# Kernel optimization log

Measured on AMD Instinct MI355X. Metric: run time of the kernel, lower is better.

Reference implementation:

```python
import jax, jax.numpy as jnp
import numpy as np

K = 3      # fixed 3x3 kernel in module
PAD = 1    # padding=1, stride=1, dilation=1, groups=1, deformable_groups=1


def _conv2d(x, w, b=None, pad=PAD):
    out = jax.lax.conv_general_dilated(
        x, w, window_strides=(1, 1), padding=((pad, pad), (pad, pad)),
        dimension_numbers=('NCHW', 'OIHW', 'NCHW'))
    if b is not None:
        out = out + b[None, :, None, None]
    return out


def _bilinear_gather(x, py, px):
    # x: [B,C,H,W]; py,px: [B,KK,H,W] float sampling coords (zero-pad outside)
    B, C, H, W = x.shape
    y0 = jnp.floor(py)
    x0 = jnp.floor(px)
    wy1 = py - y0
    wx1 = px - x0
    wy0 = 1.0 - wy1
    wx0 = 1.0 - wx1
    y0i = y0.astype(jnp.int32)
    x0i = x0.astype(jnp.int32)
    xf = x.reshape(B, C, H * W)

    def corner(yi, xi, w):
        valid = (yi >= 0) & (yi < H) & (xi >= 0) & (xi < W)
        yc = jnp.clip(yi, 0, H - 1)
        xc = jnp.clip(xi, 0, W - 1)
        idx = (yc * W + xc).reshape(B, -1)                     # [B, KK*H*W]
        v = jnp.take_along_axis(xf, idx[:, None, :], axis=2)  # [B, C, KK*H*W]
        return v * (w * valid).reshape(B, 1, -1)

    out = (corner(y0i,     x0i,     wy0 * wx0)
         + corner(y0i,     x0i + 1, wy0 * wx1)
         + corner(y0i + 1, x0i,     wy1 * wx0)
         + corner(y0i + 1, x0i + 1, wy1 * wx1))
    KK = py.shape[1]
    return out.reshape(B, C, KK, H, W)


def _deform_forward(x, offset_w, offset_b, conv_w):
    B, C, H, W = x.shape
    # offset branch: plain 3x3 conv -> [B, 2*K*K, H, W], layout (k, (dy,dx))
    off = _conv2d(x, offset_w, offset_b).reshape(B, K * K, 2, H, W)
    ys = jnp.arange(H, dtype=x.dtype)
    xs = jnp.arange(W, dtype=x.dtype)
    ky, kx = jnp.meshgrid(jnp.arange(K), jnp.arange(K), indexing='ij')
    ky = ky.reshape(-1).astype(x.dtype)   # [9]
    kx = kx.reshape(-1).astype(x.dtype)
    # sampling coords p = p0 + p_k + offset   -> [B, 9, H, W]
    py = ys[None, None, :, None] - PAD + ky[None, :, None, None] + off[:, :, 0]
    px = xs[None, None, None, :] - PAD + kx[None, :, None, None] + off[:, :, 1]
    sampled = _bilinear_gather(x, py, px)                       # [B,C,9,H,W]
    O = conv_w.shape[0]
    return jnp.einsum('bckhw,ock->bohw', sampled, conv_w.reshape(O, C, K * K))


def setup_inputs() -> dict:
    key = jax.random.key(0)
    k1, k2, k3 = jax.random.split(key, 3)
    B, C, O, H, W = 8, 256, 256, 64, 64
    x = jax.random.normal(k1, (B, C, H, W), dtype=jnp.float32)
    # small random offset weights so learned offsets are ~ +/- 2 px
    offset_w = jax.random.normal(k2, (2 * K * K, C, K, K), dtype=jnp.float32) * 0.05
    offset_b = jnp.zeros((2 * K * K,), dtype=jnp.float32)
    conv_w = jax.random.normal(k3, (O, C, K, K), dtype=jnp.float32) * 0.02
    return {"x": x, "offset_w": offset_w, "offset_b": offset_b, "conv_w": conv_w}


def reference(x, offset_w, offset_b, conv_w):
    return _deform_forward(x, offset_w, offset_b, conv_w)
```

## Files before the change

kernel.cpp:

```cpp
#include <hip/hip_runtime.h>

using short8 = __attribute__((ext_vector_type(8))) short;
using f32x4  = __attribute__((ext_vector_type(4))) float;

__device__ inline unsigned short f2bf(float f) {
  unsigned u = __float_as_uint(f);
  u += 0x7fffu + ((u >> 16) & 1u);
  return (unsigned short)(u >> 16);
}
__device__ inline float bf2f(short s) {
  return __uint_as_float(((unsigned)(unsigned short)s) << 16);
}

__device__ inline void barrier_lgkm() {
  asm volatile("s_waitcnt lgkmcnt(0)\n\ts_barrier" ::: "memory");
}

__global__ __launch_bounds__(256) void prep_all(
    const float* __restrict__ x, const float* __restrict__ cw,
    const float* __restrict__ ow, unsigned short* __restrict__ xT,
    unsigned short* __restrict__ xTlo, unsigned short* __restrict__ wBt2,
    unsigned short* __restrict__ wOt, unsigned short* __restrict__ wOtLo) {
  __shared__ float tile[32 * 268];
  int bid = blockIdx.x, tid = threadIdx.x;
  if (bid < 1024) {
    int xh = bid & 1, y = (bid >> 1) & 63, b = bid >> 7;
    int xc = tid & 31, cq = tid >> 5;
#pragma unroll 4
    for (int i = 0; i < 32; ++i) {
      int c = i * 8 + cq;
      tile[xc * 268 + c] =
          x[(((size_t)((b << 8) + c)) << 12) + (y << 6) + xh * 32 + xc];
    }
    __syncthreads();
#pragma unroll 2
    for (int i = 0; i < 8; ++i) {
      int u = i * 256 + tid;
      int site = u >> 6, c4 = u & 63;
      float4 v = *(const float4*)(tile + site * 268 + c4 * 4);
      ushort4 hi, lo;
      hi.x = f2bf(v.x); lo.x = f2bf(v.x - bf2f(hi.x));
      hi.y = f2bf(v.y); lo.y = f2bf(v.y - bf2f(hi.y));
      hi.z = f2bf(v.z); lo.z = f2bf(v.z - bf2f(hi.z));
      hi.w = f2bf(v.w); lo.w = f2bf(v.w - bf2f(hi.w));
      size_t addr = (((size_t)((b << 12) + (y << 6) + xh * 32 + site)) << 8) + c4 * 4;
      *(ushort4*)(xT + addr) = hi;
      *(ushort4*)(xTlo + addr) = lo;
    }
  } else if (bid < 3328) {
    int e = (bid - 1024) * 256 + tid;
    int kc = e & 31, o = (e >> 5) & 255, ks = e >> 13;
    int c = (ks & 7) * 32 + kc, kt = ks >> 3;
    wBt2[e] = f2bf(cw[(size_t)(o * 256 + c) * 9 + kt]);
  } else {
    int e = (bid - 3328) * 256 + tid;
    int kc = e & 31, o = (e >> 5) & 31, ks = e >> 10;
    int c = (ks & 7) * 32 + kc, kt = ks >> 3;
    float v = (o < 18) ? ow[(size_t)(o * 256 + c) * 9 + kt] : 0.f;
    unsigned short hi = f2bf(v);
    wOt[e] = hi;
    wOtLo[e] = f2bf(v - bf2f(hi));
  }
}

__device__ inline void gatherOff2(const unsigned short* xT, const unsigned short* xTlo,
                                  const unsigned short* zp, int b, int h, int p16,
                                  int q, int ccg, int ky, int kx,
                                  short8* gh, short8* gl) {
  int y = h + ky - 1;
  bool yv = (unsigned)y < 64u;
  int yc = min(max(y, 0), 63);
#pragma unroll
  for (int i = 0; i < 4; ++i) {
    int px = i * 16 + p16;
    int xx = px + kx - 1;
    bool v = yv && ((unsigned)xx < 64u);
    int xc = min(max(xx, 0), 63);
    size_t base = (((size_t)((b << 12) + (yc << 6) + xc)) << 8) + ccg * 32 + q * 8;
    const unsigned short* ph = v ? (xT + base) : zp;
    const unsigned short* pl = v ? (xTlo + base) : zp;
    gh[i] = *(const short8*)ph;
    gl[i] = *(const short8*)pl;
  }
}
__device__ inline void loadBOff2(const unsigned short* wOt, const unsigned short* wOtLo,
                                 int ks, int m16, int quad, short8* bh, short8* bl) {
  const unsigned short* bp = wOt + (ks << 10) + m16 * 32 + quad * 8;
  const unsigned short* bq = wOtLo + (ks << 10) + m16 * 32 + quad * 8;
  bh[0] = *(const short8*)bp;  bh[1] = *(const short8*)(bp + 512);
  bl[0] = *(const short8*)bq;  bl[1] = *(const short8*)(bq + 512);
}

__global__ __launch_bounds__(64) void offset_conv3(
    const unsigned short* __restrict__ xT, const unsigned short* __restrict__ xTlo,
    const unsigned short* __restrict__ wOt, const unsigned short* __restrict__ wOtLo,
    const unsigned short* __restrict__ zp, float* out) {
  __shared__ unsigned short Ah[2 * 2560], Al[2 * 2560];
  int lane = threadIdx.x;
  int bid = blockIdx.x;
  int b = bid & 7, h = (bid >> 3) & 63, ccq = bid >> 9;
  int m16 = lane & 15, quad = lane >> 4;
  int p16 = lane >> 2, q = lane & 3;
  f32x4 acc[4][2];
#pragma unroll
  for (int mt = 0; mt < 4; ++mt)
#pragma unroll
    for (int j = 0; j < 2; ++j) acc[mt][j] = (f32x4){0.f, 0.f, 0.f, 0.f};

  short8 gh[4], gl[4], bh[2], bl[2];
  gatherOff2(xT, xTlo, zp, b, h, p16, q, ccq, 0, 0, gh, gl);
  loadBOff2(wOt, wOtLo, ccq, m16, quad, bh, bl);

  for (int it = 0; it < 9; ++it) {
    int buf = it & 1;
#pragma unroll
    for (int i = 0; i < 4; ++i) {
      int px = i * 16 + p16;
      *(short8*)(Ah + buf * 2560 + px * 40 + q * 8) = gh[i];
      *(short8*)(Al + buf * 2560 + px * 40 + q * 8) = gl[i];
    }
    int jn = (it < 8) ? it + 1 : 8;
    int kyn = jn / 3, kxn = jn - kyn * 3;
    short8 ghn[4], gln[4], bhn[2], bln[2];
    loadBOff2(wOt, wOtLo, jn * 8 + ccq, m16, quad, bhn, bln);
    gatherOff2(xT, xTlo, zp, b, h, p16, q, ccq, kyn, kxn, ghn, gln);
#pragma unroll
    for (int mt = 0; mt < 4; ++mt) {
      short8 ah = *(const short8*)(Ah + buf * 2560 + (mt * 16 + m16) * 40 + quad * 8);
      short8 al = *(const short8*)(Al + buf * 2560 + (mt * 16 + m16) * 40 + quad * 8);
#pragma unroll
      for (int j = 0; j < 2; ++j) {
        acc[mt][j] = __builtin_amdgcn_mfma_f32_16x16x32_bf16(ah, bh[j], acc[mt][j], 0, 0, 0);
        acc[mt][j] = __builtin_amdgcn_mfma_f32_16x16x32_bf16(al, bh[j], acc[mt][j], 0, 0, 0);
        acc[mt][j] = __builtin_amdgcn_mfma_f32_16x16x32_bf16(ah, bl[j], acc[mt][j], 0, 0, 0);
      }
    }
#pragma unroll
    for (int i = 0; i < 4; ++i) { gh[i] = ghn[i]; gl[i] = gln[i]; }
    bh[0] = bhn[0]; bh[1] = bhn[1]; bl[0] = bln[0]; bl[1] = bln[1];
  }
#pragma unroll
  for (int j = 0; j < 2; ++j) {
    int o = j * 16 + m16;
    if (o < 18) {
      float* po = out + (((size_t)((b << 8) + 100 + ccq * 18 + o)) << 12) + (h << 6);
#pragma unroll
      for (int mt = 0; mt < 4; ++mt)
#pragma unroll
        for (int rr = 0; rr < 4; ++rr)
          po[mt * 16 + quad * 4 + rr] = acc[mt][j][rr];
    }
  }
}

__device__ inline void gather4(const unsigned short* __restrict__ xT,
                               int bbase, int q, int jt,
                               const int2* cif2, const float4* cwf4,
                               int px, short8* g, float4& wq) {
  int cc = jt / 9, kt = jt - cc * 9;
  int2 si = cif2[kt * 64 + px];
  wq = cwf4[kt * 64 + px];
  const unsigned short* base = xT + (size_t)(unsigned)(bbase + cc * 32 + q * 8);
  g[0] = *(const short8*)(base + si.x);
  g[1] = *(const short8*)(base + si.x + 256);
  g[2] = *(const short8*)(base + si.y);
  g[3] = *(const short8*)(base + si.y + 256);
}
__device__ inline void loadB(const unsigned short* __restrict__ wBt2, int wave,
                             int m16, int quad, int jt, short8* bf) {
  int cc = jt / 9, kt = jt - cc * 9;
  int ks = kt * 8 + cc;
  const unsigned short* bp =
      wBt2 + ((size_t)ks << 13) + (wave << 11) + m16 * 32 + quad * 8;
#pragma unroll
  for (int j = 0; j < 4; ++j)
    bf[j] = *(const short8*)(bp + j * 512);
}

__global__ __launch_bounds__(256, 2) void deform_main(
    const unsigned short* __restrict__ xT, const float* __restrict__ offb,
    const unsigned short* __restrict__ wBt2, float* out) {
  __shared__ float4 smem4[1504];
  char* smem = (char*)smem4;
  float4* cwf4 = (float4*)smem;
  int2*   cif2 = (int2*)(smem + 9216);
  unsigned short* At = (unsigned short*)(smem + 13824);

  int tid = threadIdx.x, lane = tid & 63, wave = tid >> 6;
  int b = blockIdx.x & 7, h = blockIdx.x >> 3;

  size_t bb = ((size_t)(b << 8)) << 12;
  for (int it = tid; it < 576; it += 256) {
    int k = it >> 6, px = it & 63;
    int ky = k / 3, kx = k - ky * 3;
    int idx = (h << 6) + px;
    float dy = offb[2 * k], dx = offb[2 * k + 1];
#pragma unroll
    for (int qq = 0; qq < 8; ++qq) {
      dy += out[bb + (((size_t)(100 + qq * 18 + 2 * k)) << 12) + idx];
      dx += out[bb + (((size_t)(101 + qq * 18 + 2 * k)) << 12) + idx];
    }
    float py = (float)(h - 1 + ky) + dy;
    float pxx = (float)(px - 1 + kx) + dx;
    float y0f = floorf(py), x0f = floorf(pxx);
    int y0 = (int)y0f, x0 = (int)x0f;
    float wy1 = py - y0f, wx1 = pxx - x0f;
    int xb; float wxl, wxr;
    if (x0 >= 0 && x0 <= 62)      { xb = x0; wxl = 1.f - wx1; wxr = wx1; }
    else if (x0 == -1)            { xb = 0;  wxl = wx1;       wxr = 0.f; }
    else if (x0 == 63)            { xb = 62; wxl = 0.f;       wxr = 1.f - wx1; }
    else                          { xb = 0;  wxl = 0.f;       wxr = 0.f; }
    float wy0v = ((unsigned)y0 < 64u) ? (1.f - wy1) : 0.f;
    float wy1v = ((unsigned)(y0 + 1) < 64u) ? wy1 : 0.f;
    int yc0 = min(max(y0, 0), 63), yc1 = min(max(y0 + 1, 0), 63);
    cwf4[it] = make_float4(wy0v * wxl, wy0v * wxr, wy1v * wxl, wy1v * wxr);
    cif2[it] = make_int2(((yc0 << 6) + xb) << 8, ((yc1 << 6) + xb) << 8);
  }
  __syncthreads();

  int m16 = lane & 15, quad = lane >> 4;
  int px = wave * 16 + (lane >> 2);
  int q  = lane & 3;
  int bbase = b << 20;
  f32x4 acc[4][4];
#pragma unroll
  for (int i = 0; i < 4; ++i)
#pragma unroll
    for (int j = 0; j < 4; ++j) acc[i][j] = (f32x4){0.f, 0.f, 0.f, 0.f};

  short8 g[4]; float4 wq; short8 bcur[4];
  gather4(xT, bbase, q, 0, cif2, cwf4, px, g, wq);
  loadB(wBt2, wave, m16, quad, 0, bcur);

  for (int it = 0; it < 72; ++it) {
    int buf = it & 1;
    short8 av;
#pragma unroll
    for (int i = 0; i < 8; ++i) {
      float v = wq.x * bf2f(g[0][i]) + wq.y * bf2f(g[1][i]) +
                wq.z * bf2f(g[2][i]) + wq.w * bf2f(g[3][i]);
      av[i] = (short)f2bf(v);
    }
    *(short8*)(At + buf * 2560 + px * 40 + q * 8) = av;
    int jn = (it < 71) ? it + 1 : 71;
    short8 bnext[4], gn[4]; float4 wqn;
    loadB(wBt2, wave, m16, quad, jn, bnext);
    gather4(xT, bbase, q, jn, cif2, cwf4, px, gn, wqn);
    barrier_lgkm();
    short8 af[4];
#pragma unroll
    for (int mt = 0; mt < 4; ++mt)
      af[mt] = *(const short8*)(At + buf * 2560 + (mt * 16 + m16) * 40 + quad * 8);
#pragma unroll
    for (int mt = 0; mt < 4; ++mt)
#pragma unroll
      for (int j = 0; j < 4; ++j)
        acc[mt][j] = __builtin_amdgcn_mfma_f32_16x16x32_bf16(af[mt], bcur[j],
                                                             acc[mt][j], 0, 0, 0);
#pragma unroll
    for (int i = 0; i < 4; ++i) g[i] = gn[i];
    wq = wqn;
#pragma unroll
    for (int j = 0; j < 4; ++j) bcur[j] = bnext[j];
  }

#pragma unroll
  for (int j = 0; j < 4; ++j) {
    int o = wave * 64 + j * 16 + m16;
    float* po = out + (((size_t)((b << 8) + o)) << 12) + (h << 6) + quad * 4;
#pragma unroll
    for (int mt = 0; mt < 4; ++mt) {
      float4 v = make_float4(acc[mt][j][0], acc[mt][j][1], acc[mt][j][2],
                             acc[mt][j][3]);
      *(float4*)(po + mt * 16) = v;
    }
  }
}

extern "C" void kernel_launch(void* const* d_in, const int* in_sizes, int n_in,
                              void* d_out, int out_size, void* d_ws, size_t ws_size,
                              hipStream_t stream) {
  const float* x     = (const float*)d_in[0];
  const float* offw  = (const float*)d_in[1];
  const float* offb  = (const float*)d_in[2];
  const float* convw = (const float*)d_in[3];
  float* out = (float*)d_out;

  char* ws = (char*)d_ws;
  unsigned short* wOt   = (unsigned short*)ws;
  unsigned short* wOtLo = (unsigned short*)(ws + 147456);
  unsigned short* wBt2  = (unsigned short*)(ws + 294912);
  unsigned short* xT    = (unsigned short*)(ws + 1474560);
  unsigned short* xTlo  = (unsigned short*)(ws + 18251776);
  const unsigned short* zp = wOt + 768;

  prep_all<<<3616, 256, 0, stream>>>(x, convw, offw, xT, xTlo, wBt2, wOt, wOtLo);
  offset_conv3<<<4096, 64, 0, stream>>>(xT, xTlo, wOt, wOtLo, zp, out);
  deform_main<<<512, 256, 0, stream>>>(xT, offb, wBt2, out);
}
```

Before: 185.5 us.

## Restructure offset conv to stage input rows in LDS and reduce channel splits in-block

```diff
diff --git a/kernel.cpp b/kernel.cpp
--- a/kernel.cpp
+++ b/kernel.cpp
@@ -63,26 +63,6 @@
   }
 }
 
-__device__ inline void gatherOff2(const unsigned short* xT, const unsigned short* xTlo,
-                                  const unsigned short* zp, int b, int h, int p16,
-                                  int q, int ccg, int ky, int kx,
-                                  short8* gh, short8* gl) {
-  int y = h + ky - 1;
-  bool yv = (unsigned)y < 64u;
-  int yc = min(max(y, 0), 63);
-#pragma unroll
-  for (int i = 0; i < 4; ++i) {
-    int px = i * 16 + p16;
-    int xx = px + kx - 1;
-    bool v = yv && ((unsigned)xx < 64u);
-    int xc = min(max(xx, 0), 63);
-    size_t base = (((size_t)((b << 12) + (yc << 6) + xc)) << 8) + ccg * 32 + q * 8;
-    const unsigned short* ph = v ? (xT + base) : zp;
-    const unsigned short* pl = v ? (xTlo + base) : zp;
-    gh[i] = *(const short8*)ph;
-    gl[i] = *(const short8*)pl;
-  }
-}
 __device__ inline void loadBOff2(const unsigned short* wOt, const unsigned short* wOtLo,
                                  int ks, int m16, int quad, short8* bh, short8* bl) {
   const unsigned short* bp = wOt + (ks << 10) + m16 * 32 + quad * 8;
@@ -91,64 +71,98 @@
   bl[0] = *(const short8*)bq;  bl[1] = *(const short8*)(bq + 512);
 }
 
-__global__ __launch_bounds__(64) void offset_conv3(
+__global__ __launch_bounds__(256) void offset_conv4(
     const unsigned short* __restrict__ xT, const unsigned short* __restrict__ xTlo,
     const unsigned short* __restrict__ wOt, const unsigned short* __restrict__ wOtLo,
-    const unsigned short* __restrict__ zp, float* out) {
-  __shared__ unsigned short Ah[2 * 2560], Al[2 * 2560];
-  int lane = threadIdx.x;
+    float* out) {
+  __shared__ unsigned short S[4 * 2 * 7920];
+  int tid = threadIdx.x, lane = tid & 63, wave = tid >> 6;
   int bid = blockIdx.x;
-  int b = bid & 7, h = (bid >> 3) & 63, ccq = bid >> 9;
+  int b = bid & 7, h = bid >> 3;
   int m16 = lane & 15, quad = lane >> 4;
-  int p16 = lane >> 2, q = lane & 3;
+  unsigned short* Sw = S + wave * 15840;
+
+  {
+    short8 z = (short8){0, 0, 0, 0, 0, 0, 0, 0};
+    if (lane < 48) {
+      int j = lane & 3, r = lane >> 2;
+      int buf = r >= 6; int rr = r - buf * 6; int ky = rr >> 1, pad = rr & 1;
+      int pxp = pad ? 65 : 0;
+      *(short8*)(Sw + buf * 7920 + (ky * 66 + pxp) * 40 + j * 8) = z;
+    }
+  }
+
   f32x4 acc[4][2];
 #pragma unroll
   for (int mt = 0; mt < 4; ++mt)
 #pragma unroll
     for (int j = 0; j < 2; ++j) acc[mt][j] = (f32x4){0.f, 0.f, 0.f, 0.f};
 
-  short8 gh[4], gl[4], bh[2], bl[2];
-  gatherOff2(xT, xTlo, zp, b, h, p16, q, ccq, 0, 0, gh, gl);
-  loadBOff2(wOt, wOtLo, ccq, m16, quad, bh, bl);
-
-  for (int it = 0; it < 9; ++it) {
-    int buf = it & 1;
-#pragma unroll
-    for (int i = 0; i < 4; ++i) {
-      int px = i * 16 + p16;
-      *(short8*)(Ah + buf * 2560 + px * 40 + q * 8) = gh[i];
-      *(short8*)(Al + buf * 2560 + px * 40 + q * 8) = gl[i];
-    }
-    int jn = (it < 8) ? it + 1 : 8;
-    int kyn = jn / 3, kxn = jn - kyn * 3;
-    short8 ghn[4], gln[4], bhn[2], bln[2];
-    loadBOff2(wOt, wOtLo, jn * 8 + ccq, m16, quad, bhn, bln);
-    gatherOff2(xT, xTlo, zp, b, h, p16, q, ccq, kyn, kxn, ghn, gln);
-#pragma unroll
-    for (int mt = 0; mt < 4; ++mt) {
-      short8 ah = *(const short8*)(Ah + buf * 2560 + (mt * 16 + m16) * 40 + quad * 8);
-      short8 al = *(const short8*)(Al + buf * 2560 + (mt * 16 + m16) * 40 + quad * 8);
-#pragma unroll
-      for (int j = 0; j < 2; ++j) {
-        acc[mt][j] = __builtin_amdgcn_mfma_f32_16x16x32_bf16(ah, bh[j], acc[mt][j], 0, 0, 0);
-        acc[mt][j] = __builtin_amdgcn_mfma_f32_16x16x32_bf16(al, bh[j], acc[mt][j], 0, 0, 0);
-        acc[mt][j] = __builtin_amdgcn_mfma_f32_16x16x32_bf16(ah, bl[j], acc[mt][j], 0, 0, 0);
+  for (int ci = 0; ci < 2; ++ci) {
+    int cc = wave + ci * 4;
+#pragma unroll
+    for (int ky = 0; ky < 3; ++ky) {
+      int y = h + ky - 1;
+      unsigned short* dh = Sw + (ky * 66 + lane + 1) * 40;
+      unsigned short* dl = dh + 7920;
+      if ((unsigned)y < 64u) {
+        size_t base = (((size_t)((b << 12) + (y << 6) + lane)) << 8) + cc * 32;
+        const unsigned short* sh_ = xT + base;
+        const unsigned short* sl_ = xTlo + base;
+#pragma unroll
+        for (int j = 0; j < 4; ++j) {
+          *(short8*)(dh + j * 8) = *(const short8*)(sh_ + j * 8);
+          *(short8*)(dl + j * 8) = *(const short8*)(sl_ + j * 8);
+        }
+      } else {
+        short8 z = (short8){0, 0, 0, 0, 0, 0, 0, 0};
+#pragma unroll
+        for (int j = 0; j < 4; ++j) {
+          *(short8*)(dh + j * 8) = z;
+          *(short8*)(dl + j * 8) = z;
+        }
       }
     }
-#pragma unroll
-    for (int i = 0; i < 4; ++i) { gh[i] = ghn[i]; gl[i] = gln[i]; }
-    bh[0] = bhn[0]; bh[1] = bhn[1]; bl[0] = bln[0]; bl[1] = bln[1];
-  }
+    for (int kt = 0; kt < 9; ++kt) {
+      int ky = kt / 3, kx = kt - ky * 3;
+      short8 bh[2], bl[2];
+      loadBOff2(wOt, wOtLo, kt * 8 + cc, m16, quad, bh, bl);
+#pragma unroll
+      for (int mt = 0; mt < 4; ++mt) {
+        const unsigned short* ap = Sw + (ky * 66 + mt * 16 + m16 + kx) * 40 + quad * 8;
+        short8 ah = *(const short8*)ap;
+        short8 al = *(const short8*)(ap + 7920);
+#pragma unroll
+        for (int j = 0; j < 2; ++j) {
+          acc[mt][j] = __builtin_amdgcn_mfma_f32_16x16x32_bf16(ah, bh[j], acc[mt][j], 0, 0, 0);
+          acc[mt][j] = __builtin_amdgcn_mfma_f32_16x16x32_bf16(al, bh[j], acc[mt][j], 0, 0, 0);
+          acc[mt][j] = __builtin_amdgcn_mfma_f32_16x16x32_bf16(ah, bl[j], acc[mt][j], 0, 0, 0);
+        }
+      }
+    }
+  }
+
+  __syncthreads();
+  float* red = (float*)S;
+#pragma unroll
+  for (int mt = 0; mt < 4; ++mt)
+#pragma unroll
+    for (int j = 0; j < 2; ++j)
+      *(f32x4*)(red + ((((wave * 4 + mt) * 2) + j) * 64 + lane) * 4) = acc[mt][j];
+  __syncthreads();
 #pragma unroll
   for (int j = 0; j < 2; ++j) {
     int o = j * 16 + m16;
+    f32x4 s = (f32x4){0.f, 0.f, 0.f, 0.f};
+#pragma unroll
+    for (int wv = 0; wv < 4; ++wv) {
+      f32x4 v = *(const f32x4*)(red + ((((wv * 4 + wave) * 2) + j) * 64 + lane) * 4);
+      s[0] += v[0]; s[1] += v[1]; s[2] += v[2]; s[3] += v[3];
+    }
     if (o < 18) {
-      float* po = out + (((size_t)((b << 8) + 100 + ccq * 18 + o)) << 12) + (h << 6);
-#pragma unroll
-      for (int mt = 0; mt < 4; ++mt)
-#pragma unroll
-        for (int rr = 0; rr < 4; ++rr)
-          po[mt * 16 + quad * 4 + rr] = acc[mt][j][rr];
+      float* po = out + (((size_t)((b << 8) + 100 + o)) << 12) + (h << 6) +
+                  wave * 16 + quad * 4;
+      *(float4*)po = make_float4(s[0], s[1], s[2], s[3]);
     }
   }
 }
@@ -194,12 +208,8 @@
     int k = it >> 6, px = it & 63;
     int ky = k / 3, kx = k - ky * 3;
     int idx = (h << 6) + px;
-    float dy = offb[2 * k], dx = offb[2 * k + 1];
-#pragma unroll
-    for (int qq = 0; qq < 8; ++qq) {
-      dy += out[bb + (((size_t)(100 + qq * 18 + 2 * k)) << 12) + idx];
-      dx += out[bb + (((size_t)(101 + qq * 18 + 2 * k)) << 12) + idx];
-    }
+    float dy = offb[2 * k]     + out[bb + (((size_t)(100 + 2 * k)) << 12) + idx];
+    float dx = offb[2 * k + 1] + out[bb + (((size_t)(101 + 2 * k)) << 12) + idx];
     float py = (float)(h - 1 + ky) + dy;
     float pxx = (float)(px - 1 + kx) + dx;
     float y0f = floorf(py), x0f = floorf(pxx);
@@ -292,9 +302,8 @@
   unsigned short* wBt2  = (unsigned short*)(ws + 294912);
   unsigned short* xT    = (unsigned short*)(ws + 1474560);
   unsigned short* xTlo  = (unsigned short*)(ws + 18251776);
-  const unsigned short* zp = wOt + 768;
 
   prep_all<<<3616, 256, 0, stream>>>(x, convw, offw, xT, xTlo, wBt2, wOt, wOtLo);
-  offset_conv3<<<4096, 64, 0, stream>>>(xT, xTlo, wOt, wOtLo, zp, out);
+  offset_conv4<<<512, 256, 0, stream>>>(xT, xTlo, wOt, wOtLo, out);
   deform_main<<<512, 256, 0, stream>>>(xT, offb, wBt2, out);
 }
```

Result: slower. 189.5 us (+2.2%).
